# Kernel optimization log

Measured on AMD Instinct MI355X. Metric: run time of the kernel, lower is better.

Reference implementation:

```python
import jax, jax.numpy as jnp
import numpy as np


def _euclidean_distances(X):
    # X: [nb_features, n_coord_rows]; pairwise euclidean distances between rows.
    sq = jnp.sum(jnp.square(X), axis=1)          # [F]
    d = -2.0 * (X @ X.T)                          # [F, F]
    d = d + sq[None, :] + sq[:, None]
    d = jnp.maximum(d, 0.0)
    return jnp.sqrt(d)


def setup_inputs() -> dict:
    key = jax.random.key(0)
    k1, k2 = jax.random.split(key)
    xs = jax.random.normal(k1, (1024, 4096), dtype=jnp.float32)
    coordinates = jax.random.normal(k2, (256, 4096), dtype=jnp.float32)
    return {"xs": xs, "coordinates": coordinates, "nb_neighbors": 16}


def reference(xs, coordinates, nb_neighbors):
    # dist over feature columns: transpose so rows are features
    dist = _euclidean_distances(coordinates.T)                # [F, F]
    _, neighbor_indexes = jax.lax.top_k(-dist, nb_neighbors)  # [F, k]
    flat_idx = neighbor_indexes.reshape(-1)                   # row-major (feature, neighbor) order
    expanded_xs = xs[:, flat_idx]                             # [B, F*k]
    expanded_coordinates = coordinates[:, flat_idx]           # [N, F*k]
    expanded_xs = expanded_xs[:, None, :, None]               # [B, 1, F*k, 1]
    expanded_coordinates = expanded_coordinates[:, None, :, None]
    return (expanded_xs, expanded_coordinates)
```

## Files before the change

### kernel.cpp

```cpp
#include <hip/hip_runtime.h>

#define NPTS 4096
#define DIM  256
#define NNB  16
#define NCAND 32
#define LTOP  8
#define JC    8
#define JPC   (NPTS / JC)
#define NSTR  (JC * 4)
#define NPART (NSTR * LTOP)

using bf16x8 = __attribute__((ext_vector_type(8))) short;
using f32x4  = __attribute__((ext_vector_type(4))) float;

static __device__ __forceinline__ unsigned short f2bf(float f) {
    unsigned u = __float_as_uint(f);
    u += 0x7FFFu + ((u >> 16) & 1u);
    return (unsigned short)(u >> 16);
}

static __device__ __forceinline__ unsigned long long packki(float k, int j) {
    unsigned u = __float_as_uint(k);
    u ^= ((unsigned)((int)u >> 31)) | 0x80000000u;
    return ((unsigned long long)u << 32) | (unsigned)j;
}

__global__ __launch_bounds__(256) void prep_kernel(const float* __restrict__ C,
                                                   float* __restrict__ Ct,
                                                   unsigned short* __restrict__ CbT,
                                                   float* __restrict__ sq) {
    __shared__ float T[64][65];
    __shared__ float sqp[4][64];
    const int t  = threadIdx.x;
    const int p0 = blockIdx.x * 64;
    const int r  = t >> 4;
    const int c4 = (t & 15) * 4;
    const int pp = t & 63;
    const int q  = t >> 6;
    float part = 0.0f;
    for (int d0 = 0; d0 < DIM; d0 += 64) {
        __syncthreads();
        #pragma unroll
        for (int s = 0; s < 4; ++s) {
            int dl = r + s * 16;
            float4 v = *(const float4*)&C[(size_t)(d0 + dl) * NPTS + p0 + c4];
            T[dl][c4 + 0] = v.x; T[dl][c4 + 1] = v.y;
            T[dl][c4 + 2] = v.z; T[dl][c4 + 3] = v.w;
        }
        __syncthreads();
        #pragma unroll
        for (int s = 0; s < 4; ++s) {
            int pl = r + s * 16;
            float4 v;
            v.x = T[c4 + 0][pl]; v.y = T[c4 + 1][pl];
            v.z = T[c4 + 2][pl]; v.w = T[c4 + 3][pl];
            *(float4*)&Ct[(size_t)(p0 + pl) * DIM + d0 + c4] = v;
            unsigned lo = (unsigned)f2bf(v.x) | ((unsigned)f2bf(v.y) << 16);
            unsigned hi = (unsigned)f2bf(v.z) | ((unsigned)f2bf(v.w) << 16);
            *(uint2*)&CbT[(size_t)(p0 + pl) * DIM + d0 + c4] = make_uint2(lo, hi);
        }
        #pragma unroll
        for (int dd = 0; dd < 16; ++dd) {
            float v = T[q * 16 + dd][pp];
            part = fmaf(v, v, part);
        }
    }
    sqp[q][pp] = part;
    __syncthreads();
    if (t < 64)
        sq[p0 + t] = ((sqp[0][t] + sqp[1][t]) + sqp[2][t]) + sqp[3][t];
}

__global__ __launch_bounds__(256) void gemm_select_kernel(
    const unsigned short* __restrict__ CbT, const float* __restrict__ sq,
    unsigned long long* __restrict__ parts)
{
    const int t    = threadIdx.x;
    const int wave = t >> 6, lane = t & 63;
    const int i0   = blockIdx.y * 64 + wave * 16;
    const int jbase = blockIdx.x * JPC;
    const int lm   = lane & 15;
    const int g    = lane >> 4;
    const int kg   = g * 8;

    bf16x8 bfr[8];
    #pragma unroll
    for (int k0 = 0; k0 < 8; ++k0)
        bfr[k0] = *(const bf16x8*)&CbT[(size_t)(i0 + lm) * DIM + k0 * 32 + kg];

    float kk[LTOP]; int jj[LTOP];
    #pragma unroll
    for (int p = 0; p < LTOP; ++p) { kk[p] = __builtin_inff(); jj[p] = 0x7FFFFFFF; }

    bf16x8 a[8], an[8];
    #pragma unroll
    for (int k0 = 0; k0 < 8; ++k0)
        a[k0] = *(const bf16x8*)&CbT[(size_t)(jbase + lm) * DIM + k0 * 32 + kg];

    for (int jt = 0; jt < JPC / 16; ++jt) {
        const int j0 = jbase + jt * 16;
        if (jt + 1 < JPC / 16) {
            #pragma unroll
            for (int k0 = 0; k0 < 8; ++k0)
                an[k0] = *(const bf16x8*)&CbT[(size_t)(j0 + 16 + lm) * DIM + k0 * 32 + kg];
        }
        f32x4 acc0 = {}, acc1 = {};
        #pragma unroll
        for (int k0 = 0; k0 < 8; k0 += 2) {
            acc0 = __builtin_amdgcn_mfma_f32_16x16x32_bf16(a[k0],     bfr[k0],     acc0, 0, 0, 0);
            acc1 = __builtin_amdgcn_mfma_f32_16x16x32_bf16(a[k0 + 1], bfr[k0 + 1], acc1, 0, 0, 0);
        }
        float4 sj = *(const float4*)&sq[j0 + g * 4];
        #pragma unroll
        for (int r = 0; r < 4; ++r) {
            float gsum = acc0[r] + acc1[r];
            float k = fmaf(-2.0f, gsum, (r == 0) ? sj.x : (r == 1) ? sj.y : (r == 2) ? sj.z : sj.w);
            int   j = j0 + g * 4 + r;
            if (k < kk[LTOP - 1]) {
                bool b[LTOP];
                #pragma unroll
                for (int p = 0; p < LTOP; ++p) b[p] = k < kk[p];
                #pragma unroll
                for (int p = LTOP - 1; p >= 1; --p) {
                    kk[p] = b[p - 1] ? kk[p - 1] : (b[p] ? k : kk[p]);
                    jj[p] = b[p - 1] ? jj[p - 1] : (b[p] ? j : jj[p]);
                }
                kk[0] = b[0] ? k : kk[0];
                jj[0] = b[0] ? j : jj[0];
            }
        }
        #pragma unroll
        for (int k0 = 0; k0 < 8; ++k0) a[k0] = an[k0];
    }

    const int row = i0 + lm;
    unsigned long long* dst = &parts[((size_t)row * NSTR + blockIdx.x * 4 + g) * LTOP];
    #pragma unroll
    for (int p = 0; p < LTOP; ++p) dst[p] = packki(kk[p], jj[p]);
}

__global__ __launch_bounds__(NPART) void merge_refine_kernel(
    const unsigned long long* __restrict__ parts, const float* __restrict__ Ct,
    int* __restrict__ fidx)
{
    __shared__ unsigned long long e[NPART];
    __shared__ float  xi[DIM];
    __shared__ int    cidx[NCAND];
    __shared__ double pd[NCAND][8];
    __shared__ double sums[NCAND];
    const int row = blockIdx.x;
    const int t   = threadIdx.x;

    unsigned long long mine = parts[(size_t)row * NPART + t];
    e[t] = mine;
    if (t < 64) *(float4*)&xi[t * 4] = *(const float4*)&Ct[(size_t)row * DIM + t * 4];
    __syncthreads();
    int rank = 0;
    for (int o = 0; o < NPART; ++o) rank += e[o] < mine;
    if (rank < NCAND) cidx[rank] = (int)(mine & 0xFFFFFFFFu);
    __syncthreads();

    if (t < NCAND * 8) {
        const int c = t >> 3, sl = t & 7;
        const int j = cidx[c];
        const float* xj = &Ct[(size_t)j * DIM];
        double s = 0.0;
        for (int d = sl * 32; d < sl * 32 + 32; d += 4) {
            float4 v = *(const float4*)&xj[d];
            double e0 = (double)xi[d + 0] - (double)v.x; s = fma(e0, e0, s);
            double e1 = (double)xi[d + 1] - (double)v.y; s = fma(e1, e1, s);
            double e2 = (double)xi[d + 2] - (double)v.z; s = fma(e2, e2, s);
            double e3 = (double)xi[d + 3] - (double)v.w; s = fma(e3, e3, s);
        }
        pd[c][sl] = s;
    }
    __syncthreads();
    if (t < NCAND) {
        double s = 0.0;
        #pragma unroll
        for (int sl = 0; sl < 8; ++sl) s += pd[t][sl];
        sums[t] = s;
    }
    __syncthreads();
    if (t < NCAND) {
        double s = sums[t]; int j = cidx[t];
        int rk = 0;
        #pragma unroll
        for (int o = 0; o < NCAND; ++o) {
            double os = sums[o]; int oj = cidx[o];
            rk += (os < s) || (os == s && oj < j);
        }
        if (rk < NNB) fidx[row * NNB + rk] = j;
    }
}

__global__ __launch_bounds__(256) void gather_all_kernel(const float* __restrict__ xs,
                                                         const float* __restrict__ coords,
                                                         const int* __restrict__ fidx,
                                                         float* __restrict__ out) {
    __shared__ float row[NPTS];
    const int rb    = blockIdx.y;
    const int slice = blockIdx.x;
    const int t     = threadIdx.x;
    const float* srow;
    float* drow;
    if (rb < 1024) { srow = xs + (size_t)rb * NPTS;            drow = out + (size_t)rb * 65536; }
    else           { srow = coords + (size_t)(rb - 1024) * NPTS;
                     drow = out + (size_t)1024 * 65536 + (size_t)(rb - 1024) * 65536; }
    const int cbase = slice * 32768;

    int4 ids[8];
    #pragma unroll
    for (int q = 0; q < 8; ++q)
        ids[q] = *(const int4*)&fidx[cbase + (q * 256 + t) * 4];

    #pragma unroll
    for (int s = 0; s < NPTS / 1024; ++s)
        *(float4*)&row[(s * 256 + t) * 4] = *(const float4*)&srow[(s * 256 + t) * 4];
    __syncthreads();

    for (int g = 0; g < 4; ++g) {
        int4 nxt[8];
        if (g < 3) {
            #pragma unroll
            for (int q = 0; q < 8; ++q)
                nxt[q] = *(const int4*)&fidx[cbase + ((g + 1) * 2048 + q * 256 + t) * 4];
        }
        #pragma unroll
        for (int q = 0; q < 8; ++q) {
            int c4 = cbase + (g * 2048 + q * 256 + t) * 4;
            int4 id = ids[q];
            f32x4 v;
            v[0] = row[id.x]; v[1] = row[id.y]; v[2] = row[id.z]; v[3] = row[id.w];
            *(f32x4*)&drow[c4] = v;
        }
        #pragma unroll
        for (int q = 0; q < 8; ++q) ids[q] = nxt[q];
    }
}

extern "C" void kernel_launch(void* const* d_in, const int* in_sizes, int n_in,
                              void* d_out, int out_size, void* d_ws, size_t ws_size,
                              hipStream_t stream) {
    const float* xs     = (const float*)d_in[0];
    const float* coords = (const float*)d_in[1];
    float* out = (float*)d_out;

    unsigned long long* parts = (unsigned long long*)out;
    float*          Ct    = out + (size_t)NPTS * NPART * 2;
    unsigned short* CbT   = (unsigned short*)(Ct + (size_t)NPTS * DIM);
    float*          sqv   = (float*)(CbT + (size_t)NPTS * DIM);
    int*            fidx  = (int*)d_ws;

    prep_kernel<<<64, 256, 0, stream>>>(coords, Ct, CbT, sqv);
    gemm_select_kernel<<<dim3(JC, 64), 256, 0, stream>>>(CbT, sqv, parts);
    merge_refine_kernel<<<NPTS, NPART, 0, stream>>>(parts, Ct, fidx);
    gather_all_kernel<<<dim3(2, 1280), 256, 0, stream>>>(xs, coords, fidx, out);
}
```

Before: 166.0 us.

## Pack distance key and index into 32-bit word and double column split

Each candidate is now encoded as one 32-bit word: the top 20 bits of the order-preserving float key plus a 12-bit column index. Top-8 insertion becomes an unconditional branchless min/max bubble in place of a guarded shift over separate key and index arrays. The number of column chunks goes from 8 to 16, which raises grid parallelism and doubles the per-row partial list, while the merge kernel ranks 32-bit values instead of 64-bit ones. Truncating the key lowers its precision, so ties among near-equal distances may pick different candidates. The larger merge block also makes the O(n^2) rank loop cost more.

After: 204.5 us. 23.2% more time.

```diff
diff --git a/kernel.cpp b/kernel.cpp
--- a/kernel.cpp
+++ b/kernel.cpp
@@ -5,7 +5,7 @@
 #define NNB  16
 #define NCAND 32
 #define LTOP  8
-#define JC    8
+#define JC    16
 #define JPC   (NPTS / JC)
 #define NSTR  (JC * 4)
 #define NPART (NSTR * LTOP)
@@ -19,10 +19,9 @@
     return (unsigned short)(u >> 16);
 }
 
-static __device__ __forceinline__ unsigned long long packki(float k, int j) {
+static __device__ __forceinline__ unsigned fbits(float k) {
     unsigned u = __float_as_uint(k);
-    u ^= ((unsigned)((int)u >> 31)) | 0x80000000u;
-    return ((unsigned long long)u << 32) | (unsigned)j;
+    return u ^ (((unsigned)((int)u >> 31)) | 0x80000000u);
 }
 
 __global__ __launch_bounds__(256) void prep_kernel(const float* __restrict__ C,
@@ -73,7 +72,7 @@
 
 __global__ __launch_bounds__(256) void gemm_select_kernel(
     const unsigned short* __restrict__ CbT, const float* __restrict__ sq,
-    unsigned long long* __restrict__ parts)
+    unsigned* __restrict__ parts)
 {
     const int t    = threadIdx.x;
     const int wave = t >> 6, lane = t & 63;
@@ -88,9 +87,9 @@
     for (int k0 = 0; k0 < 8; ++k0)
         bfr[k0] = *(const bf16x8*)&CbT[(size_t)(i0 + lm) * DIM + k0 * 32 + kg];
 
-    float kk[LTOP]; int jj[LTOP];
-    #pragma unroll
-    for (int p = 0; p < LTOP; ++p) { kk[p] = __builtin_inff(); jj[p] = 0x7FFFFFFF; }
+    unsigned kk[LTOP];
+    #pragma unroll
+    for (int p = 0; p < LTOP; ++p) kk[p] = 0xFFFFFFFFu;
 
     bf16x8 a[8], an[8];
     #pragma unroll
@@ -116,17 +115,12 @@
             float gsum = acc0[r] + acc1[r];
             float k = fmaf(-2.0f, gsum, (r == 0) ? sj.x : (r == 1) ? sj.y : (r == 2) ? sj.z : sj.w);
             int   j = j0 + g * 4 + r;
-            if (k < kk[LTOP - 1]) {
-                bool b[LTOP];
-                #pragma unroll
-                for (int p = 0; p < LTOP; ++p) b[p] = k < kk[p];
-                #pragma unroll
-                for (int p = LTOP - 1; p >= 1; --p) {
-                    kk[p] = b[p - 1] ? kk[p - 1] : (b[p] ? k : kk[p]);
-                    jj[p] = b[p - 1] ? jj[p - 1] : (b[p] ? j : jj[p]);
-                }
-                kk[0] = b[0] ? k : kk[0];
-                jj[0] = b[0] ? j : jj[0];
+            unsigned c = (fbits(k) & 0xFFFFF000u) | (unsigned)j;
+            #pragma unroll
+            for (int p = 0; p < LTOP; ++p) {
+                unsigned lo = (kk[p] < c) ? kk[p] : c;
+                c = (kk[p] < c) ? c : kk[p];
+                kk[p] = lo;
             }
         }
         #pragma unroll
@@ -134,16 +128,16 @@
     }
 
     const int row = i0 + lm;
-    unsigned long long* dst = &parts[((size_t)row * NSTR + blockIdx.x * 4 + g) * LTOP];
-    #pragma unroll
-    for (int p = 0; p < LTOP; ++p) dst[p] = packki(kk[p], jj[p]);
+    unsigned* dst = &parts[((size_t)row * NSTR + blockIdx.x * 4 + g) * LTOP];
+    #pragma unroll
+    for (int p = 0; p < LTOP; ++p) dst[p] = kk[p];
 }
 
 __global__ __launch_bounds__(NPART) void merge_refine_kernel(
-    const unsigned long long* __restrict__ parts, const float* __restrict__ Ct,
+    const unsigned* __restrict__ parts, const float* __restrict__ Ct,
     int* __restrict__ fidx)
 {
-    __shared__ unsigned long long e[NPART];
+    __shared__ unsigned e[NPART];
     __shared__ float  xi[DIM];
     __shared__ int    cidx[NCAND];
     __shared__ double pd[NCAND][8];
@@ -151,13 +145,13 @@
     const int row = blockIdx.x;
     const int t   = threadIdx.x;
 
-    unsigned long long mine = parts[(size_t)row * NPART + t];
+    unsigned mine = parts[(size_t)row * NPART + t];
     e[t] = mine;
     if (t < 64) *(float4*)&xi[t * 4] = *(const float4*)&Ct[(size_t)row * DIM + t * 4];
     __syncthreads();
     int rank = 0;
     for (int o = 0; o < NPART; ++o) rank += e[o] < mine;
-    if (rank < NCAND) cidx[rank] = (int)(mine & 0xFFFFFFFFu);
+    if (rank < NCAND) cidx[rank] = (int)(mine & 0xFFFu);
     __syncthreads();
 
     if (t < NCAND * 8) {
@@ -246,8 +240,8 @@
     const float* coords = (const float*)d_in[1];
     float* out = (float*)d_out;
 
-    unsigned long long* parts = (unsigned long long*)out;
-    float*          Ct    = out + (size_t)NPTS * NPART * 2;
+    unsigned*       parts = (unsigned*)out;
+    float*          Ct    = out + (size_t)NPTS * NPART;
     unsigned short* CbT   = (unsigned short*)(Ct + (size_t)NPTS * DIM);
     float*          sqv   = (float*)(CbT + (size_t)NPTS * DIM);
     int*            fidx  = (int*)d_ws;
```
